# Kernel optimization log

Hardware: AMD Instinct MI355X
Metric: run time of the kernel (lower is better)

## Reference

```python
import jax, jax.numpy as jnp
import numpy as np

B, N, D = 4, 2048, 1024
H, DH = 16, 64
MAX_POS_EMB = 256
TOPK = 64


def setup_inputs() -> dict:
    key = jax.random.key(0)
    ks = jax.random.split(key, 8)
    s = 0.02
    inner = H * DH
    return {
        "x": jax.random.normal(ks[0], (B, N, D), jnp.float32),
        "gating_mask": jax.random.uniform(ks[1], (B, 1, N, 1), jnp.float32),
        "Wq": jax.random.normal(ks[2], (D, inner), jnp.float32) * s,
        "bq": jnp.zeros((inner,), jnp.float32),
        "Wkv": jax.random.normal(ks[3], (D, 2 * inner), jnp.float32) * s,
        "bkv": jnp.zeros((2 * inner,), jnp.float32),
        "Wo": jax.random.normal(ks[4], (inner, D), jnp.float32) * s,
        "bo": jnp.zeros((D,), jnp.float32),
        "rel_emb": jax.random.normal(ks[5], (MAX_POS_EMB, DH), jnp.float32) * s,
        "mask": jnp.ones((B, N), bool),
        "sparse_topk": TOPK,
    }


def reference(x, gating_mask, Wq, bq, Wkv, bkv, Wo, bo, rel_emb, mask, sparse_topk):
    b, n, d = x.shape
    h, dh = H, DH
    scale = dh ** -0.5
    mask_val = -jnp.finfo(x.dtype).max

    # projections -> [b, h, n, dh]
    q = (x @ Wq + bq).reshape(b, n, h, dh).transpose(0, 2, 1, 3)
    kv = x @ Wkv + bkv
    k = kv[..., : h * dh].reshape(b, n, h, dh).transpose(0, 2, 1, 3)
    v = kv[..., h * dh:].reshape(b, n, h, dh).transpose(0, 2, 1, 3)

    dots = jnp.einsum("bhid,bhjd->bhij", q, k) * scale  # [b,h,n,n]

    # relative positional bias: q . E[clip(i-j+M, 0, M-1)]
    seq = jnp.arange(n)
    dist = jnp.clip(seq[:, None] - seq[None, :] + MAX_POS_EMB, 0, MAX_POS_EMB - 1)
    qE = jnp.einsum("bhid,rd->bhir", q, rel_emb) * scale  # [b,h,n,R]
    pos_attn = jnp.take_along_axis(qE, dist[None, None, :, :], axis=-1)  # [b,h,n,n]
    dots = dots + pos_attn

    # padding mask: mask_i * mask_j
    full_mask = mask[:, None, :, None] & mask[:, None, None, :]
    dots = jnp.where(full_mask, dots, mask_val)

    # topk sparsification: keep only scores >= k-th largest per row
    top = jax.lax.top_k(dots, sparse_topk)[0]  # [b,h,n,topk]
    vk = top[..., -1:]
    dots = jnp.where(dots < vk, mask_val, dots)

    attn = jax.nn.softmax(dots, axis=-1)
    attn = attn * gating_mask

    out = jnp.einsum("bhij,bhjd->bhid", attn, v)
    out = out.transpose(0, 2, 1, 3).reshape(b, n, h * dh)
    return out @ Wo + bo
```

## Files before the change

kernel.cpp:

```cpp
#include <hip/hip_runtime.h>
#include <stdint.h>


typedef __attribute__((ext_vector_type(8))) short short8;
typedef __attribute__((ext_vector_type(4))) float floatx4;
typedef _Float16 f16x2 __attribute__((ext_vector_type(2)));

#define Bn   4
#define Nn   2048
#define Hn   16
#define BHn  (Bn*Hn)
#define DELTA 0.0025f

__device__ __forceinline__ float bf2f(unsigned short u) {
  union { unsigned int i; float f; } v; v.i = ((unsigned int)u) << 16; return v.f;
}
__device__ __forceinline__ unsigned short f2bf(float f) {
  union { float f; unsigned int i; } v; v.f = f;
  unsigned int r = v.i + 0x7fffu + ((v.i >> 16) & 1u);
  return (unsigned short)(r >> 16);
}
__device__ __forceinline__ floatx4 mfma16(short8 a, short8 b, floatx4 c) {
  return __builtin_amdgcn_mfma_f32_16x16x32_bf16(a, b, c, 0, 0, 0);
}
__device__ __forceinline__ void split2(float x, unsigned short& h, unsigned short& m) {
  h = f2bf(x);
  m = f2bf(x - bf2f(h));
}
__device__ __forceinline__ void split3(float x, unsigned short& h, unsigned short& m, unsigned short& l) {
  h = f2bf(x);
  float r = x - bf2f(h);
  m = f2bf(r);
  l = f2bf(r - bf2f(m));
}
__device__ __forceinline__ unsigned int mapf(float f) {
  union { _Float16 h; unsigned short s; } u; u.h = (_Float16)f;
  unsigned int b = (unsigned int)u.s;
  return (b & 0x8000u) ? (b ^ 0xFFFFu) : (b | 0x8000u);
}
__device__ __forceinline__ float unmapf(unsigned int c) {
  unsigned int b = (c & 0x8000u) ? (c ^ 0x8000u) : (c ^ 0xFFFFu);
  union { _Float16 h; unsigned short s; } u; u.s = (unsigned short)b;
  return (float)u.h;
}

__global__ __launch_bounds__(256)
void transpose_split3(const float* __restrict__ W,
                      unsigned short* __restrict__ T0,
                      unsigned short* __restrict__ T1,
                      unsigned short* __restrict__ T2,
                      int K, int Ncols)
{
  __shared__ float tile[32][33];
  int k0 = blockIdx.y * 32, n0 = blockIdx.x * 32;
  int tx = threadIdx.x & 31, ty = threadIdx.x >> 5;
  for (int s = 0; s < 32; s += 8)
    tile[ty + s][tx] = W[(size_t)(k0 + ty + s) * Ncols + n0 + tx];
  __syncthreads();
  for (int s = 0; s < 32; s += 8) {
    float x = tile[tx][ty + s];
    unsigned short h, m, l;
    split3(x, h, m, l);
    size_t o = (size_t)(n0 + ty + s) * K + k0 + tx;
    T0[o] = h; T1[o] = m; T2[o] = l;
  }
}

__global__ __launch_bounds__(256)
void transpose_split2(const float* __restrict__ W,
                      unsigned short* __restrict__ T0,
                      unsigned short* __restrict__ T1,
                      int K, int Ncols)
{
  __shared__ float tile[32][33];
  int k0 = blockIdx.y * 32, n0 = blockIdx.x * 32;
  int tx = threadIdx.x & 31, ty = threadIdx.x >> 5;
  for (int s = 0; s < 32; s += 8)
    tile[ty + s][tx] = W[(size_t)(k0 + ty + s) * Ncols + n0 + tx];
  __syncthreads();
  for (int s = 0; s < 32; s += 8) {
    float x = tile[tx][ty + s];
    unsigned short h, m;
    split2(x, h, m);
    size_t o = (size_t)(n0 + ty + s) * K + k0 + tx;
    T0[o] = h; T1[o] = m;
  }
}

__global__ __launch_bounds__(256)
void convert_bf16(const float* __restrict__ in, unsigned short* __restrict__ outp, int n) {
  int i = blockIdx.x * 256 + threadIdx.x;
  if (i < n) outp[i] = f2bf(in[i]);
}

__global__ __launch_bounds__(256)
void gemm_qkv(const float* __restrict__ A,
              const unsigned short* __restrict__ B0,
              const unsigned short* __restrict__ B1,
              const unsigned short* __restrict__ B2,
              const float* __restrict__ bias,
              float* __restrict__ O32,
              unsigned short* __restrict__ Oh,
              unsigned short* __restrict__ Om,
              _Float16* __restrict__ Vh,
              int K, float scale)
{
  __shared__ unsigned short lA[3][128 * 40];
  __shared__ unsigned short lB[3][128 * 40];
  const int tid = threadIdx.x;
  const int lane = tid & 63;
  const int m0 = blockIdx.y * 128, n0 = blockIdx.x * 128;
  const bool vblk = (n0 >= 1024);
  const int wid = tid >> 6, wm = wid >> 1, wn = wid & 1;
  const int fr = lane & 15, fq = lane >> 4;
  floatx4 acc[4][4] = {};

  for (int k0 = 0; k0 < K; k0 += 32) {
    __syncthreads();
    #pragma unroll
    for (int p = 0; p < 2; p++) {
      int c = tid + p * 256;
      int row = c >> 2, kc = (c & 3) * 8;
      size_t go = (size_t)(m0 + row) * K + k0 + kc;
      float4 v0 = *(const float4*)&A[go];
      float4 v1 = *(const float4*)&A[go + 4];
      union { unsigned short u[8]; uint4 q; } hh, mm, ll;
      float xs[8] = {v0.x, v0.y, v0.z, v0.w, v1.x, v1.y, v1.z, v1.w};
      #pragma unroll
      for (int e = 0; e < 8; e++) split3(xs[e], hh.u[e], mm.u[e], ll.u[e]);
      *(uint4*)&lA[0][row * 40 + kc] = hh.q;
      *(uint4*)&lA[1][row * 40 + kc] = mm.q;
      size_t bo = (size_t)(n0 + row) * K + k0 + kc;
      *(uint4*)&lB[0][row * 40 + kc] = *(const uint4*)&B0[bo];
      *(uint4*)&lB[1][row * 40 + kc] = *(const uint4*)&B1[bo];
      if (!vblk) {
        *(uint4*)&lA[2][row * 40 + kc] = ll.q;
        *(uint4*)&lB[2][row * 40 + kc] = *(const uint4*)&B2[bo];
      }
    }
    __syncthreads();
    short8 af0[4], af1[4], af2[4], bf0[4], bf1[4], bf2v[4];
    #pragma unroll
    for (int t = 0; t < 4; t++) {
      int ao = (wm * 64 + t * 16 + fr) * 40 + 8 * fq;
      int bo2 = (wn * 64 + t * 16 + fr) * 40 + 8 * fq;
      af0[t] = *(const short8*)&lA[0][ao];
      af1[t] = *(const short8*)&lA[1][ao];
      bf0[t] = *(const short8*)&lB[0][bo2];
      bf1[t] = *(const short8*)&lB[1][bo2];
      if (!vblk) {
        af2[t] = *(const short8*)&lA[2][ao];
        bf2v[t] = *(const short8*)&lB[2][bo2];
      }
    }
    #pragma unroll
    for (int mi = 0; mi < 4; mi++)
      #pragma unroll
      for (int ni = 0; ni < 4; ni++) {
        acc[mi][ni] = mfma16(af0[mi], bf0[ni], acc[mi][ni]);
        acc[mi][ni] = mfma16(af0[mi], bf1[ni], acc[mi][ni]);
        acc[mi][ni] = mfma16(af1[mi], bf0[ni], acc[mi][ni]);
        if (!vblk) {
          acc[mi][ni] = mfma16(af1[mi], bf1[ni], acc[mi][ni]);
          acc[mi][ni] = mfma16(af0[mi], bf2v[ni], acc[mi][ni]);
          acc[mi][ni] = mfma16(af2[mi], bf0[ni], acc[mi][ni]);
        }
      }
  }
  #pragma unroll
  for (int mi = 0; mi < 4; mi++)
    #pragma unroll
    for (int ni = 0; ni < 4; ni++) {
      int nl = n0 + wn * 64 + ni * 16 + fr;
      float bv = bias[nl];
      #pragma unroll
      for (int rg = 0; rg < 4; rg++) {
        int ml = m0 + wm * 64 + mi * 16 + fq * 4 + rg;
        float val = (acc[mi][ni][rg] + bv) * scale;
        int bb = ml >> 11, ii = ml & 2047;
        int hh2 = (nl & 1023) >> 6, dd = nl & 63;
        size_t idx = (((size_t)bb * Hn + hh2) * Nn + ii) * 64 + dd;
        if (!vblk) {
          O32[idx] = val;
          unsigned short h, m;
          split2(val, h, m);
          Oh[idx] = h; Om[idx] = m;
        } else {
          Vh[idx] = (_Float16)val;
        }
      }
    }
}

__global__ __launch_bounds__(256)
void gemm_out(const float* __restrict__ A,
              const unsigned short* __restrict__ B0,
              const unsigned short* __restrict__ B1,
              const float* __restrict__ bias,
              float* __restrict__ O32,
              int Ncols, int K)
{
  __shared__ unsigned short lA[2][128 * 40];
  __shared__ unsigned short lB[2][128 * 40];
  const int tid = threadIdx.x;
  const int lane = tid & 63;
  const int m0 = blockIdx.y * 128, n0 = blockIdx.x * 128;
  const int wid = tid >> 6, wm = wid >> 1, wn = wid & 1;
  const int fr = lane & 15, fq = lane >> 4;
  floatx4 acc[4][4] = {};

  for (int k0 = 0; k0 < K; k0 += 32) {
    __syncthreads();
    #pragma unroll
    for (int p = 0; p < 2; p++) {
      int c = tid + p * 256;
      int row = c >> 2, kc = (c & 3) * 8;
      size_t go = (size_t)(m0 + row) * K + k0 + kc;
      float4 v0 = *(const float4*)&A[go];
      float4 v1 = *(const float4*)&A[go + 4];
      union { unsigned short u[8]; uint4 q; } hh, mm;
      float xs[8] = {v0.x, v0.y, v0.z, v0.w, v1.x, v1.y, v1.z, v1.w};
      #pragma unroll
      for (int e = 0; e < 8; e++) split2(xs[e], hh.u[e], mm.u[e]);
      *(uint4*)&lA[0][row * 40 + kc] = hh.q;
      *(uint4*)&lA[1][row * 40 + kc] = mm.q;
      size_t bo = (size_t)(n0 + row) * K + k0 + kc;
      *(uint4*)&lB[0][row * 40 + kc] = *(const uint4*)&B0[bo];
      *(uint4*)&lB[1][row * 40 + kc] = *(const uint4*)&B1[bo];
    }
    __syncthreads();
    short8 af[2][4], bfr[2][4];
    #pragma unroll
    for (int s = 0; s < 2; s++)
      #pragma unroll
      for (int t = 0; t < 4; t++) {
        af[s][t]  = *(const short8*)&lA[s][(wm * 64 + t * 16 + fr) * 40 + 8 * fq];
        bfr[s][t] = *(const short8*)&lB[s][(wn * 64 + t * 16 + fr) * 40 + 8 * fq];
      }
    #pragma unroll
    for (int mi = 0; mi < 4; mi++)
      #pragma unroll
      for (int ni = 0; ni < 4; ni++) {
        acc[mi][ni] = mfma16(af[0][mi], bfr[0][ni], acc[mi][ni]);
        acc[mi][ni] = mfma16(af[0][mi], bfr[1][ni], acc[mi][ni]);
        acc[mi][ni] = mfma16(af[1][mi], bfr[0][ni], acc[mi][ni]);
      }
  }
  #pragma unroll
  for (int mi = 0; mi < 4; mi++)
    #pragma unroll
    for (int ni = 0; ni < 4; ni++) {
      int nl = n0 + wn * 64 + ni * 16 + fr;
      float bv = bias[nl];
      #pragma unroll
      for (int rg = 0; rg < 4; rg++) {
        int ml = m0 + wm * 64 + mi * 16 + fq * 4 + rg;
        O32[(size_t)ml * Ncols + nl] = acc[mi][ni][rg] + bv;
      }
    }
}

__global__ __launch_bounds__(1024, 8)
void attn_k(const unsigned short* __restrict__ qh,
            const unsigned short* __restrict__ qm,
            const unsigned short* __restrict__ kh,
            const unsigned short* __restrict__ km,
            const _Float16* __restrict__ vh,
            const float* __restrict__ q32,
            const float* __restrict__ k32,
            const unsigned short* __restrict__ relbf,
            const float* __restrict__ rel32,
            const float* __restrict__ gating,
            const int* __restrict__ topkp,
            float* __restrict__ inner)
{
  extern __shared__ char smem[];
  _Float16* S = (_Float16*)smem;
  _Float16* qE = (_Float16*)(smem + 65536);

  const int ib = blockIdx.x, bh = blockIdx.y;
  const int i0 = ib * 16;
  const int b = bh >> 4, h = bh & 15;
  const int tid = threadIdx.x;
  const int lane = tid & 63, w = tid >> 6;
  const int fr = lane & 15, fq = lane >> 4;
  const int topk = topkp[0];

  const size_t qoff = ((size_t)bh * Nn + i0) * 64;
  const size_t qf = qoff + (size_t)fr * 64 + 8 * fq;
  const short8 aqh0 = *(const short8*)&qh[qf];
  const short8 aqh1 = *(const short8*)&qh[qf + 32];
  const short8 aqm0 = *(const short8*)&qm[qf];
  const short8 aqm1 = *(const short8*)&qm[qf + 32];

  const size_t kbase = (size_t)bh * Nn * 64;
  #pragma unroll 1
  for (int t2 = 0; t2 < 2; t2++) {
    const int jt = w * 2 + t2;
    #pragma unroll 1
    for (int wc = 0; wc < 4; wc++) {
      const size_t kf = kbase + (size_t)(jt * 64 + wc * 16 + fr) * 64 + 8 * fq;
      short8 bh0 = *(const short8*)&kh[kf];
      short8 bh1 = *(const short8*)&kh[kf + 32];
      short8 bm0 = *(const short8*)&km[kf];
      short8 bm1 = *(const short8*)&km[kf + 32];
      floatx4 c = {};
      c = mfma16(aqh0, bh0, c); c = mfma16(aqh1, bh1, c);
      c = mfma16(aqh0, bm0, c); c = mfma16(aqh1, bm1, c);
      c = mfma16(aqm0, bh0, c); c = mfma16(aqm1, bh1, c);
      int colsw = jt * 64 + ((wc ^ fq) * 16) + fr;
      #pragma unroll
      for (int rg = 0; rg < 4; rg++)
        S[(fq * 4 + rg) * 2048 + colsw] = (_Float16)c[rg];
    }
  }

  {
    size_t rf = (size_t)(w * 16 + fr) * 64 + 8 * fq;
    short8 rb0 = *(const short8*)&relbf[rf];
    short8 rb1 = *(const short8*)&relbf[rf + 32];
    floatx4 c = {};
    c = mfma16(aqh0, rb0, c); c = mfma16(aqh1, rb1, c);
    c = mfma16(aqm0, rb0, c); c = mfma16(aqm1, rb1, c);
    int colsw = ((w ^ fq) * 16) + fr;
    #pragma unroll
    for (int rg = 0; rg < 4; rg++)
      qE[(fq * 4 + rg) * 256 + colsw] = (_Float16)c[rg];
  }
  __syncthreads();

  const int r = w;
  const int i = i0 + r;
  const int X = (r >> 2) << 4;
  _Float16* S0 = S + r * 2048;
  const _Float16* qE0 = qE + r * 256;
  union pun { unsigned int u; f16x2 h; };
  pun cAp, cCp;
  cAp.h[0] = qE0[255 ^ X]; cAp.h[1] = cAp.h[0];
  cCp.h[0] = qE0[X];       cCp.h[1] = cCp.h[0];
  const int swl = (2 * lane) ^ X;

  unsigned int kk[16];
  unsigned int mh = 0, ml = 0;
  #pragma unroll
  for (int e = 0; e < 16; e++) {
    const int jb = 128 * e;
    pun sv, ev;
    sv.u = *(const unsigned int*)&S0[jb + swl];
    if (jb + 127 <= i) ev = cAp;
    else if (jb >= i + 256) ev = cCp;
    else {
      const int j0 = jb + 2 * lane;
      int c0 = i - j0 + 256; c0 = c0 < 0 ? 0 : (c0 > 255 ? 255 : c0);
      int c1 = i - j0 + 255; c1 = c1 < 0 ? 0 : (c1 > 255 ? 255 : c1);
      ev.h[0] = qE0[c0 ^ X]; ev.h[1] = qE0[c1 ^ X];
    }
    pun rv; rv.h = sv.h + ev.h;
    unsigned int u = rv.u;
    unsigned int sgn = (u >> 15) & 0x00010001u;
    unsigned int code = u ^ (sgn * 0x7FFFu + 0x80008000u);
    kk[e] = code;
    unsigned int chi = code & 0xFFFF0000u, clo = code << 16;
    mh = mh > chi ? mh : chi;
    ml = ml > clo ? ml : clo;
  }
  unsigned int umax = (mh > ml ? mh : ml) >> 16;
  unsigned int mxu = umax, mnu = umax;
  #pragma unroll
  for (int d = 1; d < 64; d <<= 1) {
    unsigned int o1 = (unsigned int)__shfl_xor((int)mxu, d);
    unsigned int o2 = (unsigned int)__shfl_xor((int)mnu, d);
    mxu = o1 > mxu ? o1 : mxu;
    mnu = o2 < mnu ? o2 : mnu;
  }
  const float mxv = unmapf(mxu);

  unsigned int lo = mnu, hi = mxu + 1;
  #pragma unroll 1
  for (int it = 0; it < 13; it++) {
    unsigned int mid = (lo + hi) >> 1;
    int cnt = 0;
    #pragma unroll
    for (int e = 0; e < 16; e++) {
      cnt += ((kk[e] & 0xffffu) >= mid) ? 1 : 0;
      cnt += ((kk[e] >> 16) >= mid) ? 1 : 0;
    }
    #pragma unroll
    for (int d = 1; d < 64; d <<= 1) cnt += __shfl_xor(cnt, d);
    if (cnt >= topk) lo = mid; else hi = mid;
  }
  const float Cv = unmapf(hi) + 2.0f * DELTA;
  const float Lv = unmapf(lo) - 2.0f * DELTA;
  const unsigned int Cu = mapf(Cv) + 1;
  int Lsi = (int)mapf(Lv) - 1;
  const unsigned int Lu = Lsi < 0 ? 0u : (unsigned int)Lsi;

  char* sb = (char*)S0;
  unsigned int* Pk = (unsigned int*)sb;
  int*   Jc = (int*)(sb + 512);
  float* Sx = (float*)(sb + 768);
  float* P2 = (float*)(sb + 1024);
  asm volatile("" ::: "memory");
  const unsigned long long lmlt = (1ull << lane) - 1ull;

  int base = 0, mc = 0;
  #pragma unroll
  for (int t = 0; t < 32; t++) {
    unsigned int code = (t & 1) ? (kk[t >> 1] >> 16) : (kk[t >> 1] & 0xffffu);
    const int j = 2 * lane + 128 * (t >> 1) + (t & 1);
    bool dk = code >= Cu;
    bool cd = (code >= Lu) && !dk;
    unsigned long long mk = __ballot(dk);
    if (dk) { int pos = base + __popcll(mk & lmlt); Pk[pos] = (unsigned int)j | (code << 16); }
    base += __popcll(mk);
    mk = __ballot(cd);
    if (cd) { int pos = mc + __popcll(mk & lmlt); if (pos < 64) Jc[pos] = j; }
    mc += __popcll(mk);
  }
  if (mc > 64) mc = 64;
  asm volatile("" ::: "memory");

  const double qv = (double)q32[((size_t)bh * Nn + i) * 64 + lane];
  #pragma unroll 1
  for (int c2 = 0; c2 < mc; c2++) {
    int j = Jc[c2];
    int ridx = i - j + 256; ridx = ridx < 0 ? 0 : (ridx > 255 ? 255 : ridx);
    double t2 = qv * ((double)k32[((size_t)bh * Nn + j) * 64 + lane] +
                      (double)rel32[ridx * 64 + lane]);
    #pragma unroll
    for (int d = 1; d < 64; d <<= 1) t2 += __shfl_xor(t2, d);
    if (lane == 0) Sx[c2] = (float)t2;
  }
  asm volatile("" ::: "memory");

  const int need = topk - base;
  float myx = (lane < mc) ? Sx[lane] : -3.0e38f;
  int rank = 0;
  #pragma unroll 1
  for (int c2 = 0; c2 < mc; c2++) {
    float o = Sx[c2];
    rank += (o > myx || (o == myx && c2 < lane)) ? 1 : 0;
  }
  unsigned long long bm = __ballot((lane < mc) && (rank == need - 1));
  float vk = bm ? __shfl(myx, (int)__ffsll(bm) - 1) : 3.0e38f;
  bool ck = (lane < mc) && ((rank < need) || (myx == vk));
  unsigned long long km2 = __ballot(ck);
  float pb = 0.f;
  if (ck) {
    int pos = base + __popcll(km2 & lmlt);
    Pk[pos] = (unsigned int)Jc[lane];
    pb = __expf(myx - mxv);
    P2[pos] = pb;
  }
  const int nk = base + __popcll(km2);
  float ps = pb;
  #pragma unroll 1
  for (int t = lane; t < base; t += 64) {
    float val = unmapf(Pk[t] >> 16);
    float p = __expf(val - mxv);
    P2[t] = p; ps += p;
  }
  #pragma unroll
  for (int d = 1; d < 64; d <<= 1) ps += __shfl_xor(ps, d);
  const float coef = gating[(size_t)b * Nn + i] / ps;
  asm volatile("" ::: "memory");

  const _Float16* vbp = vh + (size_t)bh * Nn * 64 + lane;
  float a0 = 0.f, a1 = 0.f, a2 = 0.f, a3 = 0.f;
  int t4 = nk & ~3;
  #pragma unroll 1
  for (int t = 0; t < t4; t += 4) {
    int j0 = (int)(Pk[t] & 0xffffu), j1 = (int)(Pk[t + 1] & 0xffffu);
    int j2 = (int)(Pk[t + 2] & 0xffffu), j3 = (int)(Pk[t + 3] & 0xffffu);
    float p0 = P2[t], p1 = P2[t + 1], p2 = P2[t + 2], p3 = P2[t + 3];
    a0 += p0 * (float)vbp[(size_t)j0 * 64];
    a1 += p1 * (float)vbp[(size_t)j1 * 64];
    a2 += p2 * (float)vbp[(size_t)j2 * 64];
    a3 += p3 * (float)vbp[(size_t)j3 * 64];
  }
  #pragma unroll 1
  for (int t = t4; t < nk; t++)
    a0 += P2[t] * (float)vbp[(size_t)(Pk[t] & 0xffffu) * 64];
  inner[((size_t)b * Nn + i) * 1024 + h * 64 + lane] = (a0 + a1 + a2 + a3) * coef;
}

extern "C" void kernel_launch(void* const* d_in, const int* in_sizes, int n_in,
                              void* d_out, int out_size, void* d_ws, size_t ws_size,
                              hipStream_t stream) {
  const float* x      = (const float*)d_in[0];
  const float* gating = (const float*)d_in[1];
  const float* Wq     = (const float*)d_in[2];
  const float* bq     = (const float*)d_in[3];
  const float* Wkv    = (const float*)d_in[4];
  const float* bkv    = (const float*)d_in[5];
  const float* Wo     = (const float*)d_in[6];
  const float* bo     = (const float*)d_in[7];
  const float* rel    = (const float*)d_in[8];
  const int*   topk   = (const int*)d_in[10];
  float* out = (float*)d_out;

  char* ws = (char*)d_ws;
  size_t off = 0;
  auto alloc = [&](size_t bytes) -> void* {
    void* p = ws + off; off += (bytes + 255) & ~(size_t)255; return p;
  };
  unsigned short* Wqt0 = (unsigned short*)alloc(1024ull * 1024 * 2);
  unsigned short* Wqt1 = (unsigned short*)alloc(1024ull * 1024 * 2);
  unsigned short* Wqt2 = (unsigned short*)alloc(1024ull * 1024 * 2);
  unsigned short* Wkt0 = (unsigned short*)alloc(2048ull * 1024 * 2);
  unsigned short* Wkt1 = (unsigned short*)alloc(2048ull * 1024 * 2);
  unsigned short* Wkt2 = (unsigned short*)alloc(2048ull * 1024 * 2);
  unsigned short* Wot0 = (unsigned short*)alloc(1024ull * 1024 * 2);
  unsigned short* Wot1 = (unsigned short*)alloc(1024ull * 1024 * 2);
  unsigned short* relbf = (unsigned short*)alloc(256ull * 64 * 2);
  float* q32 = (float*)alloc((size_t)BHn * Nn * 64 * 4);
  float* k32 = (float*)alloc((size_t)BHn * Nn * 64 * 4);
  unsigned short* qhb = (unsigned short*)alloc((size_t)BHn * Nn * 64 * 2);
  unsigned short* qmb = (unsigned short*)alloc((size_t)BHn * Nn * 64 * 2);
  unsigned short* khb = (unsigned short*)alloc((size_t)BHn * Nn * 64 * 2);
  unsigned short* kmb = (unsigned short*)alloc((size_t)BHn * Nn * 64 * 2);
  _Float16* vhb = (_Float16*)alloc((size_t)BHn * Nn * 64 * 2);
  float* inner = (float*)alloc((size_t)Bn * Nn * 1024 * 4);
  if (off > ws_size) return;

  size_t shmem = 65536 + 8192;
  (void)hipFuncSetAttribute((const void*)attn_k,
                            hipFuncAttributeMaxDynamicSharedMemorySize, (int)shmem);

  transpose_split3<<<dim3(32, 32), 256, 0, stream>>>(Wq, Wqt0, Wqt1, Wqt2, 1024, 1024);
  transpose_split3<<<dim3(64, 32), 256, 0, stream>>>(Wkv, Wkt0, Wkt1, Wkt2, 1024, 2048);
  transpose_split2<<<dim3(32, 32), 256, 0, stream>>>(Wo, Wot0, Wot1, 1024, 1024);
  convert_bf16<<<dim3(64), 256, 0, stream>>>(rel, relbf, 256 * 64);

  gemm_qkv<<<dim3(8, 64), 256, 0, stream>>>(x, Wqt0, Wqt1, Wqt2, bq,
      q32, qhb, qmb, vhb, 1024, 0.125f);
  gemm_qkv<<<dim3(16, 64), 256, 0, stream>>>(x, Wkt0, Wkt1, Wkt2, bkv,
      k32, khb, kmb, vhb, 1024, 1.0f);

  attn_k<<<dim3(128, 64), 1024, shmem, stream>>>(qhb, qmb, khb, kmb, vhb,
      q32, k32, relbf, rel, gating, topk, inner);

  gemm_out<<<dim3(8, 64), 256, 0, stream>>>(inner, Wot0, Wot1, bo,
      out, 1024, 1024);
}
```

Baseline: 1.345 ms.

## Stage K tiles through LDS and count threshold hits with ballot-popcount

The QK^T score pass now loads each 64-row K tile (hi and mid bf16 parts) cooperatively into swizzled shared memory, one 16-byte chunk per thread with a register prefetch of the next tile. Eight waves then compute MFMAs from LDS instead of each wave issuing scattered global loads. The top-k bisection count replaces per-lane counting plus a shuffle reduction with wave ballots and popcount. This adds 64 block barriers per tile loop, leaves half the waves idle during compute, and raises LDS use from 72 KB to 80 KB per block, which may reduce occupancy.

```diff
diff --git a/kernel.cpp b/kernel.cpp
--- a/kernel.cpp
+++ b/kernel.cpp
@@ -276,7 +276,9 @@
 {
   extern __shared__ char smem[];
   _Float16* S = (_Float16*)smem;
-  _Float16* qE = (_Float16*)(smem + 65536);
+  unsigned short* KtH = (unsigned short*)(smem + 65536);
+  unsigned short* KtM = KtH + 4096;
+  _Float16* qE = (_Float16*)KtH;
 
   const int ib = blockIdx.x, bh = blockIdx.y;
   const int i0 = ib * 16;
@@ -293,27 +295,42 @@
   const short8 aqm0 = *(const short8*)&qm[qf];
   const short8 aqm1 = *(const short8*)&qm[qf + 32];
 
-  const size_t kbase = (size_t)bh * Nn * 64;
-  #pragma unroll 1
-  for (int t2 = 0; t2 < 2; t2++) {
-    const int jt = w * 2 + t2;
-    #pragma unroll 1
-    for (int wc = 0; wc < 4; wc++) {
-      const size_t kf = kbase + (size_t)(jt * 64 + wc * 16 + fr) * 64 + 8 * fq;
-      short8 bh0 = *(const short8*)&kh[kf];
-      short8 bh1 = *(const short8*)&kh[kf + 32];
-      short8 bm0 = *(const short8*)&km[kf];
-      short8 bm1 = *(const short8*)&km[kf + 32];
-      floatx4 c = {};
-      c = mfma16(aqh0, bh0, c); c = mfma16(aqh1, bh1, c);
-      c = mfma16(aqh0, bm0, c); c = mfma16(aqh1, bm1, c);
-      c = mfma16(aqm0, bh0, c); c = mfma16(aqm1, bh1, c);
-      int colsw = jt * 64 + ((wc ^ fq) * 16) + fr;
-      #pragma unroll
-      for (int rg = 0; rg < 4; rg++)
-        S[(fq * 4 + rg) * 2048 + colsw] = (_Float16)c[rg];
-    }
-  }
+  {
+    const int sel = tid >> 9;
+    const int row = (tid >> 3) & 63, ch = tid & 7;
+    const int dst = row * 64 + ((ch ^ (row & 7)) * 8);
+    unsigned short* T = sel ? KtM : KtH;
+    const unsigned short* src = sel ? km : kh;
+    const size_t gbase = (size_t)bh * Nn * 64 + (size_t)row * 64 + ch * 8;
+    uint4 rr = *(const uint4*)&src[gbase];
+
+    for (int jt = 0; jt < 32; jt++) {
+      __syncthreads();
+      *(uint4*)&T[dst] = rr;
+      if (jt + 1 < 32)
+        rr = *(const uint4*)&src[gbase + (size_t)(jt + 1) * 4096];
+      __syncthreads();
+      if (w < 8 && ((jt & 1) == (w >> 2))) {
+        int wc = w & 3;
+        int row16 = wc * 16 + fr, r7 = fr & 7;
+        int b0 = row16 * 64 + ((fq ^ r7) * 8);
+        int b1 = row16 * 64 + (((fq + 4) ^ r7) * 8);
+        short8 kh0 = *(const short8*)&KtH[b0];
+        short8 kh1 = *(const short8*)&KtH[b1];
+        short8 km0 = *(const short8*)&KtM[b0];
+        short8 km1 = *(const short8*)&KtM[b1];
+        floatx4 c = {};
+        c = mfma16(aqh0, kh0, c); c = mfma16(aqh1, kh1, c);
+        c = mfma16(aqh0, km0, c); c = mfma16(aqh1, km1, c);
+        c = mfma16(aqm0, kh0, c); c = mfma16(aqm1, kh1, c);
+        int colsw = jt * 64 + ((wc ^ fq) * 16) + fr;
+        #pragma unroll
+        for (int rg = 0; rg < 4; rg++)
+          S[(fq * 4 + rg) * 2048 + colsw] = (_Float16)c[rg];
+      }
+    }
+  }
+  __syncthreads();
 
   {
     size_t rf = (size_t)(w * 16 + fr) * 64 + 8 * fq;
@@ -382,11 +399,9 @@
     int cnt = 0;
     #pragma unroll
     for (int e = 0; e < 16; e++) {
-      cnt += ((kk[e] & 0xffffu) >= mid) ? 1 : 0;
-      cnt += ((kk[e] >> 16) >= mid) ? 1 : 0;
-    }
-    #pragma unroll
-    for (int d = 1; d < 64; d <<= 1) cnt += __shfl_xor(cnt, d);
+      cnt += (int)__popcll(__ballot((kk[e] >> 16) >= mid));
+      cnt += (int)__popcll(__ballot((kk[e] & 0xffffu) >= mid));
+    }
     if (cnt >= topk) lo = mid; else hi = mid;
   }
   const float Cv = unmapf(hi) + 2.0f * DELTA;
@@ -523,7 +538,7 @@
   float* inner = (float*)alloc((size_t)Bn * Nn * 1024 * 4);
   if (off > ws_size) return;
 
-  size_t shmem = 65536 + 8192;
+  size_t shmem = 65536 + 16384;
   (void)hipFuncSetAttribute((const void*)attn_k,
                             hipFuncAttributeMaxDynamicSharedMemorySize, (int)shmem);
 
```

New measurement: 1.142 ms. 1.18x faster.
